# Performance work log

Measured on AMD Instinct MI355X. Metric: run time of the kernel, lower is better.

The kernel has to match this reference:

```python
import jax, jax.numpy as jnp
import numpy as np

NUM_HEADS = 12
THETA = 10000.0

def apply_rope(x, pos, theta):
    # x: [B, H, S, d_k]; pos: [S]
    d_k = x.shape[-1]
    inv_freq = theta ** (-jnp.arange(0, d_k, 2, dtype=jnp.float32) / d_k)  # [d_k/2]
    ang = pos[:, None].astype(jnp.float32) * inv_freq[None, :]             # [S, d_k/2]
    cos, sin = jnp.cos(ang), jnp.sin(ang)
    x1, x2 = x[..., ::2], x[..., 1::2]
    out_even = x1 * cos - x2 * sin
    out_odd = x1 * sin + x2 * cos
    # interleave back to [..., d_k]
    return jnp.stack([out_even, out_odd], axis=-1).reshape(x.shape)

def setup_inputs() -> dict:
    key = jax.random.key(0)
    ks = jax.random.split(key, 5)
    B, S, D = 1, 4096, 768
    x = jax.random.normal(ks[0], (B, S, D), dtype=jnp.float32)
    scale = 0.02
    Wq = jax.random.normal(ks[1], (D, D), dtype=jnp.float32) * scale
    Wk = jax.random.normal(ks[2], (D, D), dtype=jnp.float32) * scale
    Wv = jax.random.normal(ks[3], (D, D), dtype=jnp.float32) * scale
    Wo = jax.random.normal(ks[4], (D, D), dtype=jnp.float32) * scale
    return {"x": x, "Wq": Wq, "Wk": Wk, "Wv": Wv, "Wo": Wo}

def reference(x, Wq, Wk, Wv, Wo):
    B, S, D = x.shape
    H = NUM_HEADS
    d_k = D // H
    # projections (torch Linear: y = x @ W.T, no bias)
    Q = x @ Wq.T
    K = x @ Wk.T
    V = x @ Wv.T
    # [B, S, H*d_k] -> [B, H, S, d_k]
    def split_heads(t):
        return t.reshape(B, S, H, d_k).transpose(0, 2, 1, 3)
    Q, K, V = split_heads(Q), split_heads(K), split_heads(V)
    pos = jnp.arange(S)
    Q = apply_rope(Q, pos, THETA)
    K = apply_rope(K, pos, THETA)
    scores = jnp.einsum('bhnd,bhmd->bhnm', Q, K) * (d_k ** -0.5)  # [B,H,S,S]
    causal = jnp.tril(jnp.ones((S, S), dtype=bool))
    scores = jnp.where(causal, scores, -jnp.inf)
    attn = jax.nn.softmax(scores, axis=-1)
    out = jnp.einsum('bhnm,bhmd->bhnd', attn, V)  # [B,H,S,d_k]
    out = out.transpose(0, 2, 1, 3).reshape(B, S, D)
    return out @ Wo.T
```

## Files before the change

### kernel.cpp

```cpp
#include <hip/hip_runtime.h>
#include <hip/hip_bf16.h>
#include <cstdint>

typedef __bf16 bf16x8 __attribute__((ext_vector_type(8)));
typedef float f32x4 __attribute__((ext_vector_type(4)));
typedef float f32x16 __attribute__((ext_vector_type(16)));

static constexpr int S = 4096;
static constexpr int D = 768;
static constexpr int DK = 64;

__device__ __forceinline__ unsigned short f2bf(float f) {
  unsigned u = __float_as_uint(f);
  u = (u + 0x7fffu + ((u >> 16) & 1u)) >> 16;
  return (unsigned short)u;
}

__global__ __launch_bounds__(256) void cvt5_kernel(
    const float* __restrict__ x, const float* __restrict__ wq,
    const float* __restrict__ wk, const float* __restrict__ wv,
    const float* __restrict__ wo,
    unsigned short* __restrict__ xb, unsigned short* __restrict__ wqb,
    unsigned short* __restrict__ wkb, unsigned short* __restrict__ wvb,
    unsigned short* __restrict__ wob) {
  int i = blockIdx.x * blockDim.x + threadIdx.x;
  constexpr int NX4 = (S * D) / 4;
  constexpr int NW4 = (D * D) / 4;
  const float* src;
  unsigned short* dst;
  int off;
  if (i < NX4)               { src = x;  dst = xb;  off = i; }
  else if (i < NX4 + NW4)    { src = wq; dst = wqb; off = i - NX4; }
  else if (i < NX4 + 2*NW4)  { src = wk; dst = wkb; off = i - NX4 - NW4; }
  else if (i < NX4 + 3*NW4)  { src = wv; dst = wvb; off = i - NX4 - 2*NW4; }
  else                       { src = wo; dst = wob; off = i - NX4 - 3*NW4; }
  float4 v = reinterpret_cast<const float4*>(src)[off];
  ushort4 o;
  o.x = f2bf(v.x); o.y = f2bf(v.y); o.z = f2bf(v.z); o.w = f2bf(v.w);
  reinterpret_cast<ushort4*>(dst)[off] = o;
}

__global__ __launch_bounds__(256) void ropetab_kernel(float2* __restrict__ tab) {
  int idx = blockIdx.x * blockDim.x + threadIdx.x;
  int s = idx >> 5, i = idx & 31;
  float freq = expf(-(float)(2 * i) * (9.210340371976184f / 64.0f));
  float si, c;
  sincosf((float)s * freq, &si, &c);
  tab[idx] = make_float2(c, si);
}

__global__ __launch_bounds__(256) void qkv_gemm_kernel(
    const unsigned short* __restrict__ xb,
    const unsigned short* __restrict__ Wall,
    const float2* __restrict__ tab,
    unsigned short* __restrict__ Qh,
    unsigned short* __restrict__ Kf,
    unsigned short* __restrict__ Vf) {
  __shared__ alignas(16) unsigned short At[2][128 * 64];
  __shared__ alignas(16) unsigned short Bt[2][128 * 64];

  const int t = threadIdx.x;
  const int lane = t & 63;
  const int lr = lane & 15;
  const int hi = lane >> 4;
  const int wave = t >> 6;
  const int wr = wave >> 1, wc = wave & 1;
  const int row0 = blockIdx.x * 128;
  const int n0 = blockIdx.y * 128;

  const int trow = t >> 3;
  const int tc8  = (t & 7) * 8;
  const int tsw8 = (((t & 7) ^ (trow & 7)) * 8);
  const int sx = lr & 7;

  f32x4 acc[4][4] = {};

  auto stage = [&](int buf, int k0) {
#pragma unroll
    for (int i = 0; i < 4; ++i) {
      __builtin_amdgcn_global_load_lds(
          (const __attribute__((address_space(1))) void*)(
              xb + (size_t)(row0 + trow + 32 * i) * 768 + k0 + tsw8),
          (__attribute__((address_space(3))) void*)(&At[buf][(trow + 32 * i) * 64 + tc8]),
          16, 0, 0);
      __builtin_amdgcn_global_load_lds(
          (const __attribute__((address_space(1))) void*)(
              Wall + (size_t)(n0 + trow + 32 * i) * 768 + k0 + tsw8),
          (__attribute__((address_space(3))) void*)(&Bt[buf][(trow + 32 * i) * 64 + tc8]),
          16, 0, 0);
    }
  };

  stage(0, 0);
  __syncthreads();

#pragma unroll
  for (int ts = 0; ts < 12; ++ts) {
    const int cur = ts & 1;
    if (ts + 1 < 12) stage(cur ^ 1, (ts + 1) * 64);
#pragma unroll
    for (int kk = 0; kk < 2; ++kk) {
      const int csw = ((kk * 4 + hi) ^ sx) * 8;
      bf16x8 a[4], b[4];
#pragma unroll
      for (int rf = 0; rf < 4; ++rf)
        a[rf] = *reinterpret_cast<const bf16x8*>(
            &At[cur][(wr * 64 + rf * 16 + lr) * 64 + csw]);
#pragma unroll
      for (int nf = 0; nf < 4; ++nf)
        b[nf] = *reinterpret_cast<const bf16x8*>(
            &Bt[cur][(wc * 64 + nf * 16 + lr) * 64 + csw]);
#pragma unroll
      for (int rf = 0; rf < 4; ++rf)
#pragma unroll
        for (int nf = 0; nf < 4; ++nf)
          acc[rf][nf] = __builtin_amdgcn_mfma_f32_16x16x32_bf16(a[rf], b[nf], acc[rf][nf], 0, 0, 0);
    }
    __syncthreads();
  }

  const int z = n0 / 768;

  if (z < 2) {
#pragma unroll
    for (int nf = 0; nf < 4; ++nf) {
      const int c = n0 - z * 768 + wc * 64 + nf * 16 + lr;
      const int hh = c >> 6;
      const int dk = c & 63;
      const int ii = dk >> 1;
#pragma unroll
      for (int rf = 0; rf < 4; ++rf) {
        const int jrow = row0 + wr * 64 + rf * 16 + hi * 4;
#pragma unroll
        for (int j = 0; j < 4; ++j) {
          float v = acc[rf][nf][j];
          const int s = jrow + j;
          float pv = __shfl_xor(v, 1);
          float2 cs = tab[(size_t)s * 32 + ii];
          v = (dk & 1) ? (pv * cs.y + v * cs.x) : (v * cs.x - pv * cs.y);
          if (z == 0) {
            Qh[((size_t)hh * S + s) * DK + dk] = f2bf(v * 0.18033688f);
          } else {
            const size_t koff = ((size_t)hh * 128 + (s >> 5)) * 2048 +
                                (size_t)(dk >> 4) * 512 + ((dk >> 3) & 1) * 256 +
                                (s & 31) * 8 + (dk & 7);
            Kf[koff] = f2bf(v);
          }
        }
      }
    }
  } else {
#pragma unroll
    for (int nf = 0; nf < 4; ++nf) {
      const int c = n0 - 1536 + wc * 64 + nf * 16 + lr;
      const int hh = c >> 6;
      const int dv = c & 63;
#pragma unroll
      for (int rf = 0; rf < 4; ++rf) {
        const int jrow = row0 + wr * 64 + rf * 16 + hi * 4;
#pragma unroll
        for (int j = 0; j < 4; ++j) {
          const int s = jrow + j;
          const size_t voff = ((size_t)hh * 256 + (s >> 4)) * 1024 +
                              (size_t)(dv >> 5) * 512 + (dv & 31) * 16 +
                              ((s >> 3) & 1) * 8 + (s & 7);
          Vf[voff] = f2bf(acc[rf][nf][j]);
        }
      }
    }
  }
}

__global__ __launch_bounds__(256) void attn_kernel(
    const unsigned short* __restrict__ Qh,
    const unsigned short* __restrict__ Kf,
    const unsigned short* __restrict__ Vf,
    unsigned short* __restrict__ AO) {
  const int w = blockIdx.x * 192 + blockIdx.y;
  const int h = w >> 7;
  const int qt = 127 - (w & 127);
  const int wave = threadIdx.x >> 6;
  const int lane = threadIdx.x & 63;
  const int lq = lane & 31;
  const int hi2 = lane >> 5;
  const int q0w = qt * 32;
  const int qg = q0w + lq;

  const unsigned short* Qp = Qh + ((size_t)h * S + qg) * DK + hi2 * 8;
  const unsigned short* Kfp = Kf + (size_t)h * (S * DK) + hi2 * 256 + lq * 8;
  const unsigned short* Vfp = Vf + (size_t)h * (S * DK) + lq * 16 + hi2 * 8;

  bf16x8 qf[4];
#pragma unroll
  for (int ks = 0; ks < 4; ++ks)
    qf[ks] = *reinterpret_cast<const bf16x8*>(Qp + ks * 16);

  f32x16 acc0 = {}, acc1 = {};
  float lsum[16];
#pragma unroll
  for (int r = 0; r < 16; ++r) lsum[r] = 0.f;

  const int kvmax = ((q0w + 31) >> 6) << 6;
  const int kvfirst = 64 * wave;

  bf16x8 ka[2][4];
  if (kvfirst <= kvmax) {
    const unsigned short* K0 = Kfp + ((size_t)(kvfirst >> 5)) * 2048;
#pragma unroll
    for (int tt = 0; tt < 2; ++tt)
#pragma unroll
      for (int ks = 0; ks < 4; ++ks)
        ka[tt][ks] = *reinterpret_cast<const bf16x8*>(K0 + (size_t)tt * 2048 + ks * 512);
  }

  for (int kv0 = kvfirst; kv0 <= kvmax; kv0 += 256) {
    bf16x8 vb[2][4];
#pragma unroll
    for (int dvh = 0; dvh < 2; ++dvh)
#pragma unroll
      for (int ks = 0; ks < 4; ++ks)
        vb[dvh][ks] = *reinterpret_cast<const bf16x8*>(
            Vfp + ((size_t)(kv0 >> 4) + ks) * 1024 + dvh * 512);

    f32x16 s0 = {}, s1 = {};
#pragma unroll
    for (int ks = 0; ks < 4; ++ks) {
      s0 = __builtin_amdgcn_mfma_f32_32x32x16_bf16(ka[0][ks], qf[ks], s0, 0, 0, 0);
      s1 = __builtin_amdgcn_mfma_f32_32x32x16_bf16(ka[1][ks], qf[ks], s1, 0, 0, 0);
    }

    if ((kv0 + 256) <= kvmax) {
      const unsigned short* Kn = Kfp + ((size_t)((kv0 + 256) >> 5)) * 2048;
#pragma unroll
      for (int tt = 0; tt < 2; ++tt)
#pragma unroll
        for (int ks = 0; ks < 4; ++ks)
          ka[tt][ks] = *reinterpret_cast<const bf16x8*>(Kn + (size_t)tt * 2048 + ks * 512);
    }

    if ((kv0 + 63) > q0w) {
#pragma unroll
      for (int r = 0; r < 16; ++r) {
        const int kvr = kv0 + (r & 3) + 8 * (r >> 2) + 4 * hi2;
        if (kvr > qg) s0[r] = -1e30f;
        if (kvr + 32 > qg) s1[r] = -1e30f;
      }
    }

#pragma unroll
    for (int r = 0; r < 16; ++r) {
      float e0, e1;
      asm("v_exp_f32 %0, %1" : "=v"(e0) : "v"(s0[r]));
      asm("v_exp_f32 %0, %1" : "=v"(e1) : "v"(s1[r]));
      s0[r] = e0;
      s1[r] = e1;
      lsum[r] += e0 + e1;
    }

    bf16x8 pa[4];
#pragma unroll
    for (int ks = 0; ks < 4; ++ks) {
      const int a4 = 8 * (ks & 1);
      unsigned X01, X23, Y01, Y23;
      if (ks < 2) {
        asm("v_cvt_pk_bf16_f32 %0, %1, %2" : "=v"(X01) : "v"(s0[a4 + 0]), "v"(s0[a4 + 1]));
        asm("v_cvt_pk_bf16_f32 %0, %1, %2" : "=v"(X23) : "v"(s0[a4 + 2]), "v"(s0[a4 + 3]));
        asm("v_cvt_pk_bf16_f32 %0, %1, %2" : "=v"(Y01) : "v"(s0[a4 + 4]), "v"(s0[a4 + 5]));
        asm("v_cvt_pk_bf16_f32 %0, %1, %2" : "=v"(Y23) : "v"(s0[a4 + 6]), "v"(s0[a4 + 7]));
      } else {
        asm("v_cvt_pk_bf16_f32 %0, %1, %2" : "=v"(X01) : "v"(s1[a4 + 0]), "v"(s1[a4 + 1]));
        asm("v_cvt_pk_bf16_f32 %0, %1, %2" : "=v"(X23) : "v"(s1[a4 + 2]), "v"(s1[a4 + 3]));
        asm("v_cvt_pk_bf16_f32 %0, %1, %2" : "=v"(Y01) : "v"(s1[a4 + 4]), "v"(s1[a4 + 5]));
        asm("v_cvt_pk_bf16_f32 %0, %1, %2" : "=v"(Y23) : "v"(s1[a4 + 6]), "v"(s1[a4 + 7]));
      }
      asm volatile("v_permlane32_swap_b32 %0, %1" : "+v"(X01), "+v"(Y01));
      asm volatile("v_permlane32_swap_b32 %0, %1" : "+v"(X23), "+v"(Y23));
      union { unsigned u[4]; bf16x8 v; } P;
      P.u[0] = X01; P.u[1] = X23; P.u[2] = Y01; P.u[3] = Y23;
      pa[ks] = P.v;
    }

#pragma unroll
    for (int ks = 0; ks < 4; ++ks) {
      acc0 = __builtin_amdgcn_mfma_f32_32x32x16_bf16(pa[ks], vb[0][ks], acc0, 0, 0, 0);
      acc1 = __builtin_amdgcn_mfma_f32_32x32x16_bf16(pa[ks], vb[1][ks], acc1, 0, 0, 0);
    }
  }

#pragma unroll
  for (int off = 8; off > 0; off >>= 1)
#pragma unroll
    for (int r = 0; r < 8; ++r)
      if (r < off) lsum[r] += lsum[r + off];
  const float l_ = lsum[0] + __shfl_xor(lsum[0], 32);

  __shared__ float llds[4][32];
  __shared__ float obuf[4][64][17];

  if (hi2 == 0) llds[wave][lq] = l_;

#pragma unroll
  for (int r = 0; r < 16; ++r) obuf[wave][lane][r] = acc0[r];
  __syncthreads();

  const float Ltot = llds[0][lq] + llds[1][lq] + llds[2][lq] + llds[3][lq];
  const float linv = 1.0f / Ltot;

  float v0[4];
#pragma unroll
  for (int rr = 0; rr < 4; ++rr) {
    const int r = wave * 4 + rr;
    v0[rr] = obuf[0][lane][r] + obuf[1][lane][r] + obuf[2][lane][r] + obuf[3][lane][r];
  }
  __syncthreads();

#pragma unroll
  for (int r = 0; r < 16; ++r) obuf[wave][lane][r] = acc1[r];
  __syncthreads();

#pragma unroll
  for (int rr = 0; rr < 4; ++rr) {
    const int r = wave * 4 + rr;
    const float v1 = obuf[0][lane][r] + obuf[1][lane][r] + obuf[2][lane][r] + obuf[3][lane][r];
    const int row = (r & 3) + 8 * (r >> 2) + 4 * hi2;
    const float li = __shfl(linv, row);
    const size_t s = q0w + row;
    AO[s * D + h * DK + lq]      = f2bf(v0[rr] * li);
    AO[s * D + h * DK + 32 + lq] = f2bf(v1 * li);
  }
}

__global__ __launch_bounds__(256) void oproj_kernel(
    const unsigned short* __restrict__ AO,
    const unsigned short* __restrict__ Wob,
    float* __restrict__ out) {
  __shared__ alignas(16) unsigned short At[2][128 * 64];
  __shared__ alignas(16) unsigned short Bt[2][128 * 64];

  const int t = threadIdx.x;
  const int lane = t & 63;
  const int lr = lane & 15;
  const int hi = lane >> 4;
  const int wave = t >> 6;
  const int wr = wave >> 1, wc = wave & 1;
  const int row0 = blockIdx.x * 128;
  const int n0 = blockIdx.y * 128;

  const int trow = t >> 3;
  const int tc8  = (t & 7) * 8;
  const int tsw8 = (((t & 7) ^ (trow & 7)) * 8);
  const int sx = lr & 7;

  f32x4 acc[4][4] = {};

  auto stage = [&](int buf, int k0) {
#pragma unroll
    for (int i = 0; i < 4; ++i) {
      __builtin_amdgcn_global_load_lds(
          (const __attribute__((address_space(1))) void*)(
              AO + (size_t)(row0 + trow + 32 * i) * 768 + k0 + tsw8),
          (__attribute__((address_space(3))) void*)(&At[buf][(trow + 32 * i) * 64 + tc8]),
          16, 0, 0);
      __builtin_amdgcn_global_load_lds(
          (const __attribute__((address_space(1))) void*)(
              Wob + (size_t)(n0 + trow + 32 * i) * 768 + k0 + tsw8),
          (__attribute__((address_space(3))) void*)(&Bt[buf][(trow + 32 * i) * 64 + tc8]),
          16, 0, 0);
    }
  };

  stage(0, 0);
  __syncthreads();

#pragma unroll
  for (int ts = 0; ts < 12; ++ts) {
    const int cur = ts & 1;
    if (ts + 1 < 12) stage(cur ^ 1, (ts + 1) * 64);
#pragma unroll
    for (int kk = 0; kk < 2; ++kk) {
      const int csw = ((kk * 4 + hi) ^ sx) * 8;
      bf16x8 a[4], b[4];
#pragma unroll
      for (int rf = 0; rf < 4; ++rf)
        a[rf] = *reinterpret_cast<const bf16x8*>(
            &At[cur][(wr * 64 + rf * 16 + lr) * 64 + csw]);
#pragma unroll
      for (int nf = 0; nf < 4; ++nf)
        b[nf] = *reinterpret_cast<const bf16x8*>(
            &Bt[cur][(wc * 64 + nf * 16 + lr) * 64 + csw]);
#pragma unroll
      for (int rf = 0; rf < 4; ++rf)
#pragma unroll
        for (int nf = 0; nf < 4; ++nf)
          acc[rf][nf] = __builtin_amdgcn_mfma_f32_16x16x32_bf16(a[rf], b[nf], acc[rf][nf], 0, 0, 0);
    }
    __syncthreads();
  }

#pragma unroll
  for (int rf = 0; rf < 4; ++rf) {
    const int jrow = row0 + wr * 64 + rf * 16 + hi * 4;
#pragma unroll
    for (int nf = 0; nf < 4; ++nf) {
      const int cn = n0 + wc * 64 + nf * 16 + lr;
#pragma unroll
      for (int j = 0; j < 4; ++j)
        out[(size_t)(jrow + j) * D + cn] = acc[rf][nf][j];
    }
  }
}

extern "C" void kernel_launch(void* const* d_in, const int* in_sizes, int n_in,
                              void* d_out, int out_size, void* d_ws, size_t ws_size,
                              hipStream_t stream) {
  const float* x  = (const float*)d_in[0];
  const float* Wq = (const float*)d_in[1];
  const float* Wk = (const float*)d_in[2];
  const float* Wv = (const float*)d_in[3];
  const float* Wo = (const float*)d_in[4];
  float* out = (float*)d_out;

  char* ws = (char*)d_ws;
  unsigned short* xb  = (unsigned short*)(ws + 0);
  unsigned short* Wqb = (unsigned short*)(ws + 6291456);
  unsigned short* Wkb = (unsigned short*)(ws + 7471104);
  unsigned short* Wvb = (unsigned short*)(ws + 8650752);
  unsigned short* Wob = (unsigned short*)(ws + 9830400);
  unsigned short* Qh  = (unsigned short*)(ws + 11010048);
  unsigned short* Kf  = (unsigned short*)(ws + 17301504);
  unsigned short* Vf  = (unsigned short*)(ws + 23592960);
  unsigned short* AO  = (unsigned short*)(ws + 29884416);
  float2* tab = (float2*)(ws + 29884416);

  cvt5_kernel<<<5376, 256, 0, stream>>>(x, Wq, Wk, Wv, Wo, xb, Wqb, Wkb, Wvb, Wob);
  ropetab_kernel<<<512, 256, 0, stream>>>(tab);
  qkv_gemm_kernel<<<dim3(32, 18), 256, 0, stream>>>(xb, Wqb, tab, Qh, Kf, Vf);
  attn_kernel<<<dim3(8, 192), 256, 0, stream>>>(Qh, Kf, Vf, AO);
  oproj_kernel<<<dim3(32, 6), 256, 0, stream>>>(AO, Wob, out);
}
```

Before: 107.7 us.

## Use 8-wave QKV GEMM blocks and rebalance attention block-to-work mapping

The QKV projection GEMM now launches 512 threads per block, so each of 8 waves computes a 32x64 sub-tile instead of 64x64, and the LDS staging is re-indexed per wave. This halves per-thread accumulators, which raises wave-level parallelism and helps hide latency. The attention kernel's block index now maps to (head, query-tile) pairs interleaved in groups of three heads, so each column of the grid gets a balanced mix of long and short causal tiles. The aim is better load balance across CUs, at the cost of more index arithmetic and a different cache locality pattern.

```diff
diff --git a/kernel.cpp b/kernel.cpp
--- a/kernel.cpp
+++ b/kernel.cpp
@@ -49,7 +49,7 @@
   tab[idx] = make_float2(c, si);
 }
 
-__global__ __launch_bounds__(256) void qkv_gemm_kernel(
+__global__ __launch_bounds__(512) void qkv_gemm_kernel(
     const unsigned short* __restrict__ xb,
     const unsigned short* __restrict__ Wall,
     const float2* __restrict__ tab,
@@ -67,26 +67,26 @@
   const int wr = wave >> 1, wc = wave & 1;
   const int row0 = blockIdx.x * 128;
   const int n0 = blockIdx.y * 128;
-
-  const int trow = t >> 3;
-  const int tc8  = (t & 7) * 8;
-  const int tsw8 = (((t & 7) ^ (trow & 7)) * 8);
   const int sx = lr & 7;
 
-  f32x4 acc[4][4] = {};
+  f32x4 acc[2][4] = {};
 
   auto stage = [&](int buf, int k0) {
 #pragma unroll
-    for (int i = 0; i < 4; ++i) {
+    for (int j = 0; j < 2; ++j) {
+      const int ci = wave * 128 + j * 64 + lane;
+      const int row = ci >> 3;
+      const int c16 = ci & 7;
+      const int csrc = (c16 ^ (row & 7)) * 8;
       __builtin_amdgcn_global_load_lds(
           (const __attribute__((address_space(1))) void*)(
-              xb + (size_t)(row0 + trow + 32 * i) * 768 + k0 + tsw8),
-          (__attribute__((address_space(3))) void*)(&At[buf][(trow + 32 * i) * 64 + tc8]),
+              xb + (size_t)(row0 + row) * 768 + k0 + csrc),
+          (__attribute__((address_space(3))) void*)(&At[buf][row * 64 + c16 * 8]),
           16, 0, 0);
       __builtin_amdgcn_global_load_lds(
           (const __attribute__((address_space(1))) void*)(
-              Wall + (size_t)(n0 + trow + 32 * i) * 768 + k0 + tsw8),
-          (__attribute__((address_space(3))) void*)(&Bt[buf][(trow + 32 * i) * 64 + tc8]),
+              Wall + (size_t)(n0 + row) * 768 + k0 + csrc),
+          (__attribute__((address_space(3))) void*)(&Bt[buf][row * 64 + c16 * 8]),
           16, 0, 0);
     }
   };
@@ -101,17 +101,17 @@
 #pragma unroll
     for (int kk = 0; kk < 2; ++kk) {
       const int csw = ((kk * 4 + hi) ^ sx) * 8;
-      bf16x8 a[4], b[4];
-#pragma unroll
-      for (int rf = 0; rf < 4; ++rf)
+      bf16x8 a[2], b[4];
+#pragma unroll
+      for (int rf = 0; rf < 2; ++rf)
         a[rf] = *reinterpret_cast<const bf16x8*>(
-            &At[cur][(wr * 64 + rf * 16 + lr) * 64 + csw]);
+            &At[cur][(wr * 32 + rf * 16 + lr) * 64 + csw]);
 #pragma unroll
       for (int nf = 0; nf < 4; ++nf)
         b[nf] = *reinterpret_cast<const bf16x8*>(
             &Bt[cur][(wc * 64 + nf * 16 + lr) * 64 + csw]);
 #pragma unroll
-      for (int rf = 0; rf < 4; ++rf)
+      for (int rf = 0; rf < 2; ++rf)
 #pragma unroll
         for (int nf = 0; nf < 4; ++nf)
           acc[rf][nf] = __builtin_amdgcn_mfma_f32_16x16x32_bf16(a[rf], b[nf], acc[rf][nf], 0, 0, 0);
@@ -129,8 +129,8 @@
       const int dk = c & 63;
       const int ii = dk >> 1;
 #pragma unroll
-      for (int rf = 0; rf < 4; ++rf) {
-        const int jrow = row0 + wr * 64 + rf * 16 + hi * 4;
+      for (int rf = 0; rf < 2; ++rf) {
+        const int jrow = row0 + wr * 32 + rf * 16 + hi * 4;
 #pragma unroll
         for (int j = 0; j < 4; ++j) {
           float v = acc[rf][nf][j];
@@ -156,8 +156,8 @@
       const int hh = c >> 6;
       const int dv = c & 63;
 #pragma unroll
-      for (int rf = 0; rf < 4; ++rf) {
-        const int jrow = row0 + wr * 64 + rf * 16 + hi * 4;
+      for (int rf = 0; rf < 2; ++rf) {
+        const int jrow = row0 + wr * 32 + rf * 16 + hi * 4;
 #pragma unroll
         for (int j = 0; j < 4; ++j) {
           const int s = jrow + j;
@@ -176,9 +176,21 @@
     const unsigned short* __restrict__ Kf,
     const unsigned short* __restrict__ Vf,
     unsigned short* __restrict__ AO) {
-  const int w = blockIdx.x * 192 + blockIdx.y;
-  const int h = w >> 7;
-  const int qt = 127 - (w & 127);
+  const int c = blockIdx.x;
+  const int sslot = blockIdx.y;
+  const int m3 = 3 * (c >> 1);
+  const int g = sslot / 3, r = sslot - 3 * g;
+  int h, qt;
+  if ((c & 1) == 0) {
+    if (r == 0)      { h = m3;     qt = 127 - 2 * g; }
+    else if (r == 1) { h = m3 + 1; qt = 127 - 2 * g; }
+    else             { h = m3;     qt = 126 - 2 * g; }
+  } else {
+    if (r == 0)      { h = m3 + 2; qt = 127 - 2 * g; }
+    else if (r == 1) { h = m3 + 2; qt = 126 - 2 * g; }
+    else             { h = m3 + 1; qt = 126 - 2 * g; }
+  }
+
   const int wave = threadIdx.x >> 6;
   const int lane = threadIdx.x & 63;
   const int lq = lane & 31;
@@ -198,7 +210,7 @@
   f32x16 acc0 = {}, acc1 = {};
   float lsum[16];
 #pragma unroll
-  for (int r = 0; r < 16; ++r) lsum[r] = 0.f;
+  for (int r2 = 0; r2 < 16; ++r2) lsum[r2] = 0.f;
 
   const int kvmax = ((q0w + 31) >> 6) << 6;
   const int kvfirst = 64 * wave;
@@ -240,21 +252,21 @@
 
     if ((kv0 + 63) > q0w) {
 #pragma unroll
-      for (int r = 0; r < 16; ++r) {
-        const int kvr = kv0 + (r & 3) + 8 * (r >> 2) + 4 * hi2;
-        if (kvr > qg) s0[r] = -1e30f;
-        if (kvr + 32 > qg) s1[r] = -1e30f;
+      for (int rr = 0; rr < 16; ++rr) {
+        const int kvr = kv0 + (rr & 3) + 8 * (rr >> 2) + 4 * hi2;
+        if (kvr > qg) s0[rr] = -1e30f;
+        if (kvr + 32 > qg) s1[rr] = -1e30f;
       }
     }
 
 #pragma unroll
-    for (int r = 0; r < 16; ++r) {
+    for (int rr = 0; rr < 16; ++rr) {
       float e0, e1;
-      asm("v_exp_f32 %0, %1" : "=v"(e0) : "v"(s0[r]));
-      asm("v_exp_f32 %0, %1" : "=v"(e1) : "v"(s1[r]));
-      s0[r] = e0;
-      s1[r] = e1;
-      lsum[r] += e0 + e1;
+      asm("v_exp_f32 %0, %1" : "=v"(e0) : "v"(s0[rr]));
+      asm("v_exp_f32 %0, %1" : "=v"(e1) : "v"(s1[rr]));
+      s0[rr] = e0;
+      s1[rr] = e1;
+      lsum[rr] += e0 + e1;
     }
 
     bf16x8 pa[4];
@@ -290,8 +302,8 @@
 #pragma unroll
   for (int off = 8; off > 0; off >>= 1)
 #pragma unroll
-    for (int r = 0; r < 8; ++r)
-      if (r < off) lsum[r] += lsum[r + off];
+    for (int rr = 0; rr < 8; ++rr)
+      if (rr < off) lsum[rr] += lsum[rr + off];
   const float l_ = lsum[0] + __shfl_xor(lsum[0], 32);
 
   __shared__ float llds[4][32];
@@ -300,7 +312,7 @@
   if (hi2 == 0) llds[wave][lq] = l_;
 
 #pragma unroll
-  for (int r = 0; r < 16; ++r) obuf[wave][lane][r] = acc0[r];
+  for (int rr = 0; rr < 16; ++rr) obuf[wave][lane][rr] = acc0[rr];
   __syncthreads();
 
   const float Ltot = llds[0][lq] + llds[1][lq] + llds[2][lq] + llds[3][lq];
@@ -309,20 +321,20 @@
   float v0[4];
 #pragma unroll
   for (int rr = 0; rr < 4; ++rr) {
-    const int r = wave * 4 + rr;
-    v0[rr] = obuf[0][lane][r] + obuf[1][lane][r] + obuf[2][lane][r] + obuf[3][lane][r];
+    const int rq = wave * 4 + rr;
+    v0[rr] = obuf[0][lane][rq] + obuf[1][lane][rq] + obuf[2][lane][rq] + obuf[3][lane][rq];
   }
   __syncthreads();
 
 #pragma unroll
-  for (int r = 0; r < 16; ++r) obuf[wave][lane][r] = acc1[r];
+  for (int rr = 0; rr < 16; ++rr) obuf[wave][lane][rr] = acc1[rr];
   __syncthreads();
 
 #pragma unroll
   for (int rr = 0; rr < 4; ++rr) {
-    const int r = wave * 4 + rr;
-    const float v1 = obuf[0][lane][r] + obuf[1][lane][r] + obuf[2][lane][r] + obuf[3][lane][r];
-    const int row = (r & 3) + 8 * (r >> 2) + 4 * hi2;
+    const int rq = wave * 4 + rr;
+    const float v1 = obuf[0][lane][rq] + obuf[1][lane][rq] + obuf[2][lane][rq] + obuf[3][lane][rq];
+    const int row = (rq & 3) + 8 * (rq >> 2) + 4 * hi2;
     const float li = __shfl(linv, row);
     const size_t s = q0w + row;
     AO[s * D + h * DK + lq]      = f2bf(v0[rr] * li);
@@ -434,7 +446,7 @@
 
   cvt5_kernel<<<5376, 256, 0, stream>>>(x, Wq, Wk, Wv, Wo, xb, Wqb, Wkb, Wvb, Wob);
   ropetab_kernel<<<512, 256, 0, stream>>>(tab);
-  qkv_gemm_kernel<<<dim3(32, 18), 256, 0, stream>>>(xb, Wqb, tab, Qh, Kf, Vf);
+  qkv_gemm_kernel<<<dim3(32, 18), 512, 0, stream>>>(xb, Wqb, tab, Qh, Kf, Vf);
   attn_kernel<<<dim3(8, 192), 256, 0, stream>>>(Qh, Kf, Vf, AO);
   oproj_kernel<<<dim3(32, 6), 256, 0, stream>>>(AO, Wob, out);
 }
```

Measured after the change: 100.8 us. -6.4%, faster.
